# Optimization experiments

Measured on AMD Instinct MI355X. Metric: run time of the kernel, lower is better.

The kernel has to match this reference:

```python
import math
import jax, jax.numpy as jnp
import numpy as np

B, S, D = 16, 2048, 256

def setup_inputs() -> dict:
    key = jax.random.key(0)
    kq, kk, kv, km = jax.random.split(key, 4)
    q = jax.random.normal(kq, (B, S, D), dtype=jnp.float32)
    k = jax.random.normal(kk, (B, S, D), dtype=jnp.float32)
    v = jax.random.normal(kv, (B, S, D), dtype=jnp.float32)
    mask = jax.random.randint(km, (B, S, S), 0, 2, dtype=jnp.int32)
    return {"q": q, "k": k, "v": v, "mask": mask}

def reference(q, k, v, mask):
    dim_input = q.shape[-1]
    # scores: [B, S, S]
    scores = jnp.einsum('bqd,bkd->bqk', q, k) / math.sqrt(dim_input)
    # non-standard masking: masked positions set to 0.0 (NOT -inf) before softmax
    scores = jnp.where(mask == 0, jnp.float32(0.0), scores)
    att = jax.nn.softmax(scores, axis=-1)
    # original: if mask.sum() == 0, attention is all zeros
    att = jnp.where(mask.sum() > 0, att, jnp.zeros_like(att))
    return jnp.einsum('bqk,bkd->bqd', att, v)
```

## Files before the change

### kernel.cpp

```cpp
#include <hip/hip_runtime.h>


#define B_  16
#define S_  2048
#define D_  256
#define KT  32
#define NT_ 64
#define TILE_BYTES 16384

typedef short bf16x8 __attribute__((ext_vector_type(8)));
typedef float f32x4  __attribute__((ext_vector_type(4)));

__device__ __forceinline__ unsigned short f2bf(float x) {
    union { float f; unsigned u; } c; c.f = x;
    unsigned u = c.u;
    u += 0x7FFFu + ((u >> 16) & 1u);
    return (unsigned short)(u >> 16);
}

#define GLDS(g, l) __builtin_amdgcn_global_load_lds( \
    (const __attribute__((address_space(1))) void*)(g), \
    (__attribute__((address_space(3))) void*)(l), 16, 0, 0)

__global__ void conv_k(const float* __restrict__ k, char* __restrict__ kbf) {
    const int gid = blockIdx.x * 256 + threadIdx.x;
    const int d8  = gid & 31;
    const int kv  = (gid >> 5) & 2047;
    const int b   = gid >> 16;
    const float* src = k + (((size_t)(b * S_ + kv)) << 8) + d8 * 8;
    const float4 f0 = *(const float4*)src;
    const float4 f1 = *(const float4*)(src + 4);
    bf16x8 h;
    h[0] = (short)f2bf(f0.x); h[1] = (short)f2bf(f0.y);
    h[2] = (short)f2bf(f0.z); h[3] = (short)f2bf(f0.w);
    h[4] = (short)f2bf(f1.x); h[5] = (short)f2bf(f1.y);
    h[6] = (short)f2bf(f1.z); h[7] = (short)f2bf(f1.w);
    const int tile = kv >> 5, kvl = kv & 31;
    char* dst = kbf + (((size_t)(b * NT_ + tile)) << 14)
                    + (kvl << 9) + ((d8 * 16) ^ ((kvl & 7) << 4));
    *(bf16x8*)dst = h;
}

__global__ void conv_vt(const float* __restrict__ v, char* __restrict__ vtbf) {
    const int gid  = blockIdx.x * 256 + threadIdx.x;
    const int d    = gid & 255;
    const int g    = (gid >> 8) & 3;
    const int tile = (gid >> 10) & 63;
    const int b    = gid >> 16;
    const int kv0  = tile * KT + g * 8;
    const float* src = v + (((size_t)(b * S_ + kv0)) << 8) + d;
    bf16x8 h;
    #pragma unroll
    for (int j = 0; j < 8; ++j) h[j] = (short)f2bf(src[(size_t)j << 8]);
    char* dst = vtbf + (((size_t)(b * NT_ + tile)) << 14)
                     + (d << 6) + ((g * 16) ^ (((d >> 1) & 3) << 4));
    *(bf16x8*)dst = h;
}

__global__ __launch_bounds__(256, 1)
void attn_main(const float* __restrict__ q, const int* __restrict__ mask,
               const char* __restrict__ kbf, const char* __restrict__ vtbf,
               float* __restrict__ out)
{
    __shared__ alignas(128) char lds[73728];

    const int tid  = threadIdx.x;
    const int wid  = tid >> 6;
    const int lane = tid & 63;
    const int ln15 = lane & 15;
    const int quad = lane >> 4;
    const int swzK = (ln15 & 7) << 4;
    const int swzA = ((ln15 >> 1) & 3) << 4;

    const int bid = blockIdx.x;
    const int bx  = (bid & 7) * 32 + (bid >> 3);
    const int b   = bx >> 4;
    const int qt  = bx & 15;
    const int qw  = qt * 128 + wid * 32;

    const float QS = 0.09016844f;
    bf16x8 aq[2][8];
    #pragma unroll
    for (int s = 0; s < 2; ++s) {
        const float* qrow = q + ((size_t)(b * S_ + qw + s * 16 + ln15)) * D_;
        #pragma unroll
        for (int ks = 0; ks < 8; ++ks) {
            const float4 f0 = *(const float4*)(qrow + ks * 32 + quad * 8);
            const float4 f1 = *(const float4*)(qrow + ks * 32 + quad * 8 + 4);
            bf16x8 a;
            a[0] = (short)f2bf(f0.x * QS); a[1] = (short)f2bf(f0.y * QS);
            a[2] = (short)f2bf(f0.z * QS); a[3] = (short)f2bf(f0.w * QS);
            a[4] = (short)f2bf(f1.x * QS); a[5] = (short)f2bf(f1.y * QS);
            a[6] = (short)f2bf(f1.z * QS); a[7] = (short)f2bf(f1.w * QS);
            aq[s][ks] = a;
        }
    }

    bf16x8 ones;
    #pragma unroll
    for (int e = 0; e < 8; ++e) ones[e] = (short)0x3F80;

    f32x4 oacc[2][16];
    #pragma unroll
    for (int s = 0; s < 2; ++s)
        #pragma unroll
        for (int i = 0; i < 16; ++i) oacc[s][i] = (f32x4){0.f, 0.f, 0.f, 0.f};
    f32x4 lacc[2];
    lacc[0] = (f32x4){0.f, 0.f, 0.f, 0.f};
    lacc[1] = (f32x4){0.f, 0.f, 0.f, 0.f};

    const char* ktile = kbf  + (((size_t)b * NT_) << 14);
    const char* vtile = vtbf + (((size_t)b * NT_) << 14);
    char* pw = lds + 65536 + wid * 2048;
    const int c0 = wid * 4;

    #pragma unroll
    for (int c = 0; c < 4; ++c) {
        GLDS(ktile + (c0 + c) * 1024 + lane * 16, lds +         (c0 + c) * 1024);
        GLDS(vtile + (c0 + c) * 1024 + lane * 16, lds + 32768 + (c0 + c) * 1024);
    }

    const int* mbase = mask + ((size_t)(b * S_ + qw + 4 * quad)) * S_;
    int mcur[16], mnext[16];
    #pragma unroll
    for (int s = 0; s < 2; ++s)
        #pragma unroll
        for (int nt = 0; nt < 2; ++nt)
            #pragma unroll
            for (int r = 0; r < 4; ++r)
                mcur[s * 8 + nt * 4 + r] =
                    mbase[(size_t)(s * 16 + r) * S_ + nt * 16 + ln15];

    for (int t = 0; t < NT_; ++t) {
        const int cur = t & 1;
        __syncthreads();

        if (t + 1 < NT_) {
            const char* kg = ktile + ((size_t)(t + 1) << 14);
            const char* vg = vtile + ((size_t)(t + 1) << 14);
            const int nb = cur ^ 1;
            #pragma unroll
            for (int c = 0; c < 4; ++c) {
                GLDS(kg + (c0 + c) * 1024 + lane * 16, lds + nb * 16384 +         (c0 + c) * 1024);
                GLDS(vg + (c0 + c) * 1024 + lane * 16, lds + 32768 + nb * 16384 + (c0 + c) * 1024);
            }
            const int kv2 = (t + 1) * KT;
            #pragma unroll
            for (int s = 0; s < 2; ++s)
                #pragma unroll
                for (int nt = 0; nt < 2; ++nt)
                    #pragma unroll
                    for (int r = 0; r < 4; ++r)
                        mnext[s * 8 + nt * 4 + r] =
                            mbase[(size_t)(s * 16 + r) * S_ + kv2 + nt * 16 + ln15];
        }

        const char* kl = lds + cur * 16384;
        f32x4 sacc[2][2];
        sacc[0][0] = (f32x4){0.f, 0.f, 0.f, 0.f};
        sacc[0][1] = (f32x4){0.f, 0.f, 0.f, 0.f};
        sacc[1][0] = (f32x4){0.f, 0.f, 0.f, 0.f};
        sacc[1][1] = (f32x4){0.f, 0.f, 0.f, 0.f};
        #pragma unroll
        for (int ks = 0; ks < 8; ++ks) {
            #pragma unroll
            for (int nt = 0; nt < 2; ++nt) {
                const int off = ((nt * 16 + ln15) << 9)
                              + (((ks << 6) + (quad << 4)) ^ swzK);
                const bf16x8 bk = *(const bf16x8*)(kl + off);
                sacc[0][nt] = __builtin_amdgcn_mfma_f32_16x16x32_bf16(aq[0][ks], bk, sacc[0][nt], 0, 0, 0);
                sacc[1][nt] = __builtin_amdgcn_mfma_f32_16x16x32_bf16(aq[1][ks], bk, sacc[1][nt], 0, 0, 0);
            }
        }

        #pragma unroll
        for (int s = 0; s < 2; ++s) {
            #pragma unroll
            for (int nt = 0; nt < 2; ++nt) {
                #pragma unroll
                for (int r = 0; r < 4; ++r) {
                    const float p = (mcur[s * 8 + nt * 4 + r] != 0)
                                  ? exp2f(sacc[s][nt][r]) : 1.0f;
                    const int row  = s * 16 + 4 * quad + r;
                    const int boff = (row << 6)
                                   + ((nt * 32 + ln15 * 2) ^ (((row >> 1) & 3) << 4));
                    *(unsigned short*)(pw + boff) = f2bf(p);
                }
            }
        }

        const bf16x8 ap0 = *(const bf16x8*)(pw + (ln15 << 6)        + ((quad << 4) ^ swzA));
        const bf16x8 ap1 = *(const bf16x8*)(pw + ((16 + ln15) << 6) + ((quad << 4) ^ swzA));
        lacc[0] = __builtin_amdgcn_mfma_f32_16x16x32_bf16(ap0, ones, lacc[0], 0, 0, 0);
        lacc[1] = __builtin_amdgcn_mfma_f32_16x16x32_bf16(ap1, ones, lacc[1], 0, 0, 0);
        const char* vl = lds + 32768 + cur * 16384;
        #pragma unroll
        for (int nt2 = 0; nt2 < 16; ++nt2) {
            const int voff = ((nt2 * 16 + ln15) << 6) + ((quad << 4) ^ swzA);
            const bf16x8 bv = *(const bf16x8*)(vl + voff);
            oacc[0][nt2] = __builtin_amdgcn_mfma_f32_16x16x32_bf16(ap0, bv, oacc[0][nt2], 0, 0, 0);
            oacc[1][nt2] = __builtin_amdgcn_mfma_f32_16x16x32_bf16(ap1, bv, oacc[1][nt2], 0, 0, 0);
        }

        if (t + 1 < NT_) {
            #pragma unroll
            for (int i = 0; i < 16; ++i) mcur[i] = mnext[i];
        }
    }

    #pragma unroll
    for (int s = 0; s < 2; ++s) {
        #pragma unroll
        for (int r = 0; r < 4; ++r) {
            const float inv = 1.0f / lacc[s][r];
            float* orow = out + ((size_t)(b * S_ + qw + s * 16 + 4 * quad + r)) * D_ + ln15;
            #pragma unroll
            for (int nt2 = 0; nt2 < 16; ++nt2)
                orow[nt2 * 16] = oacc[s][nt2][r] * inv;
        }
    }
}

#define QT 128
#define KTF 64
#define NW 8
#define KSTR 264
#define VSTR 72
#define PSTR 72

__global__ __launch_bounds__(512, 2)
void attn_fused_v1(const float* __restrict__ q, const float* __restrict__ k,
                   const float* __restrict__ v, const int* __restrict__ mask,
                   float* __restrict__ out)
{
    __shared__ unsigned short Kl[KTF * KSTR];
    __shared__ unsigned short Vt[D_ * VSTR];
    __shared__ unsigned short Pl[NW][16 * PSTR];

    const int tid  = threadIdx.x;
    const int wid  = tid >> 6;
    const int lane = tid & 63;
    const int ln15 = lane & 15;
    const int quad = lane >> 4;
    const int bid = blockIdx.x;
    const int bx  = (bid & 7) * 32 + (bid >> 3);
    const int b  = bx >> 4;
    const int qt = bx & 15;
    const int qw = qt * QT + wid * 16;

    const float* qb = q + ((size_t)b * S_ + qw) * D_;
    const float* kb = k + (size_t)b * S_ * D_;
    const float* vb = v + (size_t)b * S_ * D_;
    const int*   mb = mask + ((size_t)b * S_ + qw) * (size_t)S_;

    bf16x8 aq[8];
    {
        const float* qrow = qb + (size_t)ln15 * D_;
        #pragma unroll
        for (int ks = 0; ks < 8; ++ks) {
            const float4 f0 = *(const float4*)(qrow + ks * 32 + quad * 8);
            const float4 f1 = *(const float4*)(qrow + ks * 32 + quad * 8 + 4);
            bf16x8 a;
            a[0] = (short)f2bf(f0.x * 0.0625f); a[1] = (short)f2bf(f0.y * 0.0625f);
            a[2] = (short)f2bf(f0.z * 0.0625f); a[3] = (short)f2bf(f0.w * 0.0625f);
            a[4] = (short)f2bf(f1.x * 0.0625f); a[5] = (short)f2bf(f1.y * 0.0625f);
            a[6] = (short)f2bf(f1.z * 0.0625f); a[7] = (short)f2bf(f1.w * 0.0625f);
            aq[ks] = a;
        }
    }
    bf16x8 ones;
    #pragma unroll
    for (int e = 0; e < 8; ++e) ones[e] = (short)0x3F80;
    f32x4 oacc[16];
    #pragma unroll
    for (int i = 0; i < 16; ++i) oacc[i] = (f32x4){0.f, 0.f, 0.f, 0.f};
    f32x4 lacc = (f32x4){0.f, 0.f, 0.f, 0.f};
    const int kst_c0 = (tid & 63) * 4;

    for (int kt2 = 0; kt2 < S_ / KTF; ++kt2) {
        const int kvbase = kt2 * KTF;
        int mval[4][4];
        #pragma unroll
        for (int nt = 0; nt < 4; ++nt)
            #pragma unroll
            for (int r = 0; r < 4; ++r)
                mval[nt][r] = mb[(size_t)(4 * quad + r) * S_ + kvbase + nt * 16 + ln15];
        __syncthreads();
        {
            const float* ks_ = kb + (size_t)kvbase * D_;
            #pragma unroll
            for (int pass = 0; pass < 8; ++pass) {
                const int r = pass * 8 + wid;
                const float4 f = *(const float4*)(ks_ + (size_t)r * D_ + kst_c0);
                ushort4 h;
                h.x = f2bf(f.x); h.y = f2bf(f.y); h.z = f2bf(f.z); h.w = f2bf(f.w);
                *(ushort4*)&Kl[r * KSTR + kst_c0] = h;
            }
        }
        {
            const float* vs_ = vb + (size_t)kvbase * D_;
            #pragma unroll
            for (int pass = 0; pass < 8; ++pass) {
                const int idx = pass * 8 + wid;
                const int kv  = (idx & 3) * 16 + ln15;
                const int d0  = (idx >> 2) * 16 + 4 * quad;
                const float4 f = *(const float4*)(vs_ + (size_t)kv * D_ + d0);
                Vt[(d0 + 0) * VSTR + kv] = f2bf(f.x);
                Vt[(d0 + 1) * VSTR + kv] = f2bf(f.y);
                Vt[(d0 + 2) * VSTR + kv] = f2bf(f.z);
                Vt[(d0 + 3) * VSTR + kv] = f2bf(f.w);
            }
        }
        __syncthreads();
        f32x4 sacc[4];
        #pragma unroll
        for (int nt = 0; nt < 4; ++nt) sacc[nt] = (f32x4){0.f, 0.f, 0.f, 0.f};
        #pragma unroll
        for (int ks = 0; ks < 8; ++ks) {
            #pragma unroll
            for (int nt = 0; nt < 4; ++nt) {
                const bf16x8 bk =
                    *(const bf16x8*)&Kl[(nt * 16 + ln15) * KSTR + ks * 32 + quad * 8];
                sacc[nt] = __builtin_amdgcn_mfma_f32_16x16x32_bf16(aq[ks], bk, sacc[nt], 0, 0, 0);
            }
        }
        unsigned short* pwv = Pl[wid];
        #pragma unroll
        for (int nt = 0; nt < 4; ++nt) {
            #pragma unroll
            for (int r = 0; r < 4; ++r) {
                const float s = sacc[nt][r];
                const float p = (mval[nt][r] != 0) ? __expf(s) : 1.0f;
                pwv[(4 * quad + r) * PSTR + nt * 16 + ln15] = f2bf(p);
            }
        }
        #pragma unroll
        for (int ks2 = 0; ks2 < 2; ++ks2) {
            const bf16x8 ap = *(const bf16x8*)&pwv[ln15 * PSTR + ks2 * 32 + quad * 8];
            lacc = __builtin_amdgcn_mfma_f32_16x16x32_bf16(ap, ones, lacc, 0, 0, 0);
            #pragma unroll
            for (int nt2 = 0; nt2 < 16; ++nt2) {
                const bf16x8 bv =
                    *(const bf16x8*)&Vt[(nt2 * 16 + ln15) * VSTR + ks2 * 32 + quad * 8];
                oacc[nt2] = __builtin_amdgcn_mfma_f32_16x16x32_bf16(ap, bv, oacc[nt2], 0, 0, 0);
            }
        }
    }
    #pragma unroll
    for (int r = 0; r < 4; ++r) {
        const float inv = 1.0f / lacc[r];
        float* orow = out + ((size_t)b * S_ + qw + 4 * quad + r) * D_ + ln15;
        #pragma unroll
        for (int nt2 = 0; nt2 < 16; ++nt2)
            orow[nt2 * 16] = oacc[nt2][r] * inv;
    }
}

extern "C" void kernel_launch(void* const* d_in, const int* in_sizes, int n_in,
                              void* d_out, int out_size, void* d_ws, size_t ws_size,
                              hipStream_t stream) {
    const float* q    = (const float*)d_in[0];
    const float* k    = (const float*)d_in[1];
    const float* v    = (const float*)d_in[2];
    const int*   mask = (const int*)d_in[3];
    float*       out  = (float*)d_out;

    const size_t one = (size_t)B_ * NT_ * TILE_BYTES;
    if (ws_size >= 2 * one) {
        char* kbf  = (char*)d_ws;
        char* vtbf = kbf + one;
        conv_k <<<4096, 256, 0, stream>>>(k, kbf);
        conv_vt<<<4096, 256, 0, stream>>>(v, vtbf);
        attn_main<<<256, 256, 0, stream>>>(q, mask, kbf, vtbf, out);
    } else {
        attn_fused_v1<<<512, 512, 0, stream>>>(q, k, v, mask, out);
    }
}
```

Before: 182.5 us.

## Split KV across two blocks, bit-pack mask, merge prep kernels, add reduce

New measurement: 311.2 us. +70.5%, slower.

```diff
diff --git a/kernel.cpp b/kernel.cpp
--- a/kernel.cpp
+++ b/kernel.cpp
@@ -4,8 +4,8 @@
 #define B_  16
 #define S_  2048
 #define D_  256
-#define KT  32
 #define NT_ 64
+#define NPH 32
 #define TILE_BYTES 16384
 
 typedef short bf16x8 __attribute__((ext_vector_type(8)));
@@ -22,45 +22,62 @@
     (const __attribute__((address_space(1))) void*)(g), \
     (__attribute__((address_space(3))) void*)(l), 16, 0, 0)
 
-__global__ void conv_k(const float* __restrict__ k, char* __restrict__ kbf) {
-    const int gid = blockIdx.x * 256 + threadIdx.x;
-    const int d8  = gid & 31;
-    const int kv  = (gid >> 5) & 2047;
-    const int b   = gid >> 16;
-    const float* src = k + (((size_t)(b * S_ + kv)) << 8) + d8 * 8;
-    const float4 f0 = *(const float4*)src;
-    const float4 f1 = *(const float4*)(src + 4);
-    bf16x8 h;
-    h[0] = (short)f2bf(f0.x); h[1] = (short)f2bf(f0.y);
-    h[2] = (short)f2bf(f0.z); h[3] = (short)f2bf(f0.w);
-    h[4] = (short)f2bf(f1.x); h[5] = (short)f2bf(f1.y);
-    h[6] = (short)f2bf(f1.z); h[7] = (short)f2bf(f1.w);
-    const int tile = kv >> 5, kvl = kv & 31;
-    char* dst = kbf + (((size_t)(b * NT_ + tile)) << 14)
-                    + (kvl << 9) + ((d8 * 16) ^ ((kvl & 7) << 4));
-    *(bf16x8*)dst = h;
-}
-
-__global__ void conv_vt(const float* __restrict__ v, char* __restrict__ vtbf) {
-    const int gid  = blockIdx.x * 256 + threadIdx.x;
-    const int d    = gid & 255;
-    const int g    = (gid >> 8) & 3;
-    const int tile = (gid >> 10) & 63;
-    const int b    = gid >> 16;
-    const int kv0  = tile * KT + g * 8;
-    const float* src = v + (((size_t)(b * S_ + kv0)) << 8) + d;
-    bf16x8 h;
-    #pragma unroll
-    for (int j = 0; j < 8; ++j) h[j] = (short)f2bf(src[(size_t)j << 8]);
-    char* dst = vtbf + (((size_t)(b * NT_ + tile)) << 14)
-                     + (d << 6) + ((g * 16) ^ (((d >> 1) & 3) << 4));
-    *(bf16x8*)dst = h;
-}
-
-__global__ __launch_bounds__(256, 1)
-void attn_main(const float* __restrict__ q, const int* __restrict__ mask,
-               const char* __restrict__ kbf, const char* __restrict__ vtbf,
-               float* __restrict__ out)
+__global__ __launch_bounds__(256)
+void prep_all(const float* __restrict__ k, const float* __restrict__ v,
+              const int* __restrict__ mask,
+              char* __restrict__ kbf, char* __restrict__ vtbf,
+              unsigned* __restrict__ pm)
+{
+    const int bid = blockIdx.x;
+    if (bid < 4096) {
+        const int gid = bid * 256 + threadIdx.x;
+        const int d8  = gid & 31;
+        const int kv  = (gid >> 5) & 2047;
+        const int b   = gid >> 16;
+        const float* src = k + (((size_t)(b * S_ + kv)) << 8) + d8 * 8;
+        const float4 f0 = *(const float4*)src;
+        const float4 f1 = *(const float4*)(src + 4);
+        bf16x8 h;
+        h[0] = (short)f2bf(f0.x); h[1] = (short)f2bf(f0.y);
+        h[2] = (short)f2bf(f0.z); h[3] = (short)f2bf(f0.w);
+        h[4] = (short)f2bf(f1.x); h[5] = (short)f2bf(f1.y);
+        h[6] = (short)f2bf(f1.z); h[7] = (short)f2bf(f1.w);
+        const int tile = kv >> 5, kvl = kv & 31;
+        char* dst = kbf + (((size_t)(b * NT_ + tile)) << 14)
+                        + (kvl << 9) + ((d8 * 16) ^ ((kvl & 7) << 4));
+        *(bf16x8*)dst = h;
+    } else if (bid < 8192) {
+        const int gid  = (bid - 4096) * 256 + threadIdx.x;
+        const int d    = gid & 255;
+        const int g    = (gid >> 8) & 3;
+        const int tile = (gid >> 10) & 63;
+        const int b    = gid >> 16;
+        const int kv0  = tile * 32 + g * 8;
+        const float* src = v + (((size_t)(b * S_ + kv0)) << 8) + d;
+        bf16x8 h;
+        #pragma unroll
+        for (int j = 0; j < 8; ++j) h[j] = (short)f2bf(src[(size_t)j << 8]);
+        char* dst = vtbf + (((size_t)(b * NT_ + tile)) << 14)
+                         + (d << 6) + ((g * 16) ^ (((d >> 1) & 3) << 4));
+        *(bf16x8*)dst = h;
+    } else {
+        const int wave = ((bid - 8192) * 256 + (int)threadIdx.x) >> 6;
+        const int lane = threadIdx.x & 63;
+        #pragma unroll 4
+        for (int it = 0; it < 32; ++it) {
+            const size_t grp = (size_t)it * 32768 + wave;
+            const int mv = mask[grp * 64 + lane];
+            const unsigned long long bal = __ballot(mv != 0);
+            if (lane == 0)      pm[grp * 2]     = (unsigned)bal;
+            else if (lane == 1) pm[grp * 2 + 1] = (unsigned)(bal >> 32);
+        }
+    }
+}
+
+__global__ __launch_bounds__(256, 2)
+void attn_split(const float* __restrict__ q, const unsigned* __restrict__ pm,
+                const char* __restrict__ kbf, const char* __restrict__ vtbf,
+                float* __restrict__ po, float* __restrict__ pl)
 {
     __shared__ alignas(128) char lds[73728];
 
@@ -73,9 +90,10 @@
     const int swzA = ((ln15 >> 1) & 3) << 4;
 
     const int bid = blockIdx.x;
-    const int bx  = (bid & 7) * 32 + (bid >> 3);
-    const int b   = bx >> 4;
-    const int qt  = bx & 15;
+    const int bx  = (bid & 7) * 64 + (bid >> 3);
+    const int b   = bx >> 5;
+    const int qt  = (bx >> 1) & 15;
+    const int hb  = bx & 1;
     const int qw  = qt * 128 + wid * 32;
 
     const float QS = 0.09016844f;
@@ -109,116 +127,138 @@
     lacc[0] = (f32x4){0.f, 0.f, 0.f, 0.f};
     lacc[1] = (f32x4){0.f, 0.f, 0.f, 0.f};
 
-    const char* ktile = kbf  + (((size_t)b * NT_) << 14);
-    const char* vtile = vtbf + (((size_t)b * NT_) << 14);
+    const char* ktile = kbf  + ((((size_t)b * NT_ + hb * 32)) << 14);
+    const char* vtile = vtbf + ((((size_t)b * NT_ + hb * 32)) << 14);
     char* pw = lds + 65536 + wid * 2048;
-    const int c0 = wid * 4;
+    const int cc = wid * 4;
 
     #pragma unroll
     for (int c = 0; c < 4; ++c) {
-        GLDS(ktile + (c0 + c) * 1024 + lane * 16, lds +         (c0 + c) * 1024);
-        GLDS(vtile + (c0 + c) * 1024 + lane * 16, lds + 32768 + (c0 + c) * 1024);
-    }
-
-    const int* mbase = mask + ((size_t)(b * S_ + qw + 4 * quad)) * S_;
-    int mcur[16], mnext[16];
+        GLDS(ktile + (cc + c) * 1024 + lane * 16, lds +         (cc + c) * 1024);
+        GLDS(vtile + (cc + c) * 1024 + lane * 16, lds + 32768 + (cc + c) * 1024);
+    }
+
+    const unsigned* pmrow = pm + ((size_t)(b * S_ + qw + 4 * quad)) * 64 + hb * 32;
+    unsigned mcur[8], mnext[8];
     #pragma unroll
     for (int s = 0; s < 2; ++s)
         #pragma unroll
-        for (int nt = 0; nt < 2; ++nt)
-            #pragma unroll
-            for (int r = 0; r < 4; ++r)
-                mcur[s * 8 + nt * 4 + r] =
-                    mbase[(size_t)(s * 16 + r) * S_ + nt * 16 + ln15];
-
-    for (int t = 0; t < NT_; ++t) {
-        const int cur = t & 1;
-        __syncthreads();
-
-        if (t + 1 < NT_) {
-            const char* kg = ktile + ((size_t)(t + 1) << 14);
-            const char* vg = vtile + ((size_t)(t + 1) << 14);
-            const int nb = cur ^ 1;
-            #pragma unroll
-            for (int c = 0; c < 4; ++c) {
-                GLDS(kg + (c0 + c) * 1024 + lane * 16, lds + nb * 16384 +         (c0 + c) * 1024);
-                GLDS(vg + (c0 + c) * 1024 + lane * 16, lds + 32768 + nb * 16384 + (c0 + c) * 1024);
-            }
-            const int kv2 = (t + 1) * KT;
-            #pragma unroll
-            for (int s = 0; s < 2; ++s)
-                #pragma unroll
-                for (int nt = 0; nt < 2; ++nt)
-                    #pragma unroll
-                    for (int r = 0; r < 4; ++r)
-                        mnext[s * 8 + nt * 4 + r] =
-                            mbase[(size_t)(s * 16 + r) * S_ + kv2 + nt * 16 + ln15];
-        }
-
-        const char* kl = lds + cur * 16384;
-        f32x4 sacc[2][2];
-        sacc[0][0] = (f32x4){0.f, 0.f, 0.f, 0.f};
-        sacc[0][1] = (f32x4){0.f, 0.f, 0.f, 0.f};
-        sacc[1][0] = (f32x4){0.f, 0.f, 0.f, 0.f};
-        sacc[1][1] = (f32x4){0.f, 0.f, 0.f, 0.f};
-        #pragma unroll
-        for (int ks = 0; ks < 8; ++ks) {
-            #pragma unroll
-            for (int nt = 0; nt < 2; ++nt) {
-                const int off = ((nt * 16 + ln15) << 9)
-                              + (((ks << 6) + (quad << 4)) ^ swzK);
-                const bf16x8 bk = *(const bf16x8*)(kl + off);
-                sacc[0][nt] = __builtin_amdgcn_mfma_f32_16x16x32_bf16(aq[0][ks], bk, sacc[0][nt], 0, 0, 0);
-                sacc[1][nt] = __builtin_amdgcn_mfma_f32_16x16x32_bf16(aq[1][ks], bk, sacc[1][nt], 0, 0, 0);
-            }
-        }
-
-        #pragma unroll
-        for (int s = 0; s < 2; ++s) {
-            #pragma unroll
-            for (int nt = 0; nt < 2; ++nt) {
-                #pragma unroll
-                for (int r = 0; r < 4; ++r) {
-                    const float p = (mcur[s * 8 + nt * 4 + r] != 0)
-                                  ? exp2f(sacc[s][nt][r]) : 1.0f;
-                    const int row  = s * 16 + 4 * quad + r;
-                    const int boff = (row << 6)
-                                   + ((nt * 32 + ln15 * 2) ^ (((row >> 1) & 3) << 4));
-                    *(unsigned short*)(pw + boff) = f2bf(p);
-                }
-            }
-        }
-
-        const bf16x8 ap0 = *(const bf16x8*)(pw + (ln15 << 6)        + ((quad << 4) ^ swzA));
-        const bf16x8 ap1 = *(const bf16x8*)(pw + ((16 + ln15) << 6) + ((quad << 4) ^ swzA));
-        lacc[0] = __builtin_amdgcn_mfma_f32_16x16x32_bf16(ap0, ones, lacc[0], 0, 0, 0);
-        lacc[1] = __builtin_amdgcn_mfma_f32_16x16x32_bf16(ap1, ones, lacc[1], 0, 0, 0);
-        const char* vl = lds + 32768 + cur * 16384;
-        #pragma unroll
-        for (int nt2 = 0; nt2 < 16; ++nt2) {
-            const int voff = ((nt2 * 16 + ln15) << 6) + ((quad << 4) ^ swzA);
-            const bf16x8 bv = *(const bf16x8*)(vl + voff);
-            oacc[0][nt2] = __builtin_amdgcn_mfma_f32_16x16x32_bf16(ap0, bv, oacc[0][nt2], 0, 0, 0);
-            oacc[1][nt2] = __builtin_amdgcn_mfma_f32_16x16x32_bf16(ap1, bv, oacc[1][nt2], 0, 0, 0);
-        }
-
-        if (t + 1 < NT_) {
-            #pragma unroll
-            for (int i = 0; i < 16; ++i) mcur[i] = mnext[i];
-        }
-    }
+        for (int r = 0; r < 4; ++r)
+            mcur[s * 4 + r] = pmrow[(size_t)(s * 16 + r) * 64];
+
+#define PHASE_BODY(T, CUR)                                                      \
+    {                                                                           \
+        __syncthreads();                                                        \
+        if ((T) + 1 < NPH) {                                                    \
+            const char* kg_ = ktile + ((size_t)((T) + 1) << 14);                \
+            const char* vg_ = vtile + ((size_t)((T) + 1) << 14);                \
+            _Pragma("unroll")                                                   \
+            for (int c = 0; c < 4; ++c) {                                       \
+                GLDS(kg_ + (cc + c) * 1024 + lane * 16,                         \
+                     lds + (CUR ^ 1) * 16384 +         (cc + c) * 1024);        \
+                GLDS(vg_ + (cc + c) * 1024 + lane * 16,                         \
+                     lds + 32768 + (CUR ^ 1) * 16384 + (cc + c) * 1024);        \
+            }                                                                   \
+            _Pragma("unroll")                                                   \
+            for (int s = 0; s < 2; ++s)                                         \
+                _Pragma("unroll")                                               \
+                for (int r = 0; r < 4; ++r)                                     \
+                    mnext[s * 4 + r] = pmrow[(size_t)(s * 16 + r) * 64 + (T) + 1]; \
+        }                                                                       \
+        const char* kl = lds + (CUR) * 16384;                                   \
+        f32x4 sacc[2][2];                                                       \
+        sacc[0][0] = (f32x4){0.f, 0.f, 0.f, 0.f};                               \
+        sacc[0][1] = (f32x4){0.f, 0.f, 0.f, 0.f};                               \
+        sacc[1][0] = (f32x4){0.f, 0.f, 0.f, 0.f};                               \
+        sacc[1][1] = (f32x4){0.f, 0.f, 0.f, 0.f};                               \
+        __builtin_amdgcn_s_setprio(1);                                          \
+        _Pragma("unroll")                                                       \
+        for (int ks = 0; ks < 8; ++ks) {                                        \
+            _Pragma("unroll")                                                   \
+            for (int nt = 0; nt < 2; ++nt) {                                    \
+                const int off = ((nt * 16 + ln15) << 9)                         \
+                              + (((ks << 6) + (quad << 4)) ^ swzK);             \
+                const bf16x8 bk = *(const bf16x8*)(kl + off);                   \
+                sacc[0][nt] = __builtin_amdgcn_mfma_f32_16x16x32_bf16(aq[0][ks], bk, sacc[0][nt], 0, 0, 0); \
+                sacc[1][nt] = __builtin_amdgcn_mfma_f32_16x16x32_bf16(aq[1][ks], bk, sacc[1][nt], 0, 0, 0); \
+            }                                                                   \
+        }                                                                       \
+        __builtin_amdgcn_s_setprio(0);                                          \
+        _Pragma("unroll")                                                       \
+        for (int s = 0; s < 2; ++s) {                                           \
+            _Pragma("unroll")                                                   \
+            for (int nt = 0; nt < 2; ++nt) {                                    \
+                _Pragma("unroll")                                               \
+                for (int r = 0; r < 4; ++r) {                                   \
+                    const float p = ((mcur[s * 4 + r] >> (nt * 16 + ln15)) & 1u) \
+                                  ? exp2f(sacc[s][nt][r]) : 1.0f;               \
+                    const int row  = s * 16 + 4 * quad + r;                     \
+                    const int boff = (row << 6)                                 \
+                                   + ((nt * 32 + ln15 * 2) ^ (((row >> 1) & 3) << 4)); \
+                    *(unsigned short*)(pw + boff) = f2bf(p);                    \
+                }                                                               \
+            }                                                                   \
+        }                                                                       \
+        const bf16x8 ap0 = *(const bf16x8*)(pw + (ln15 << 6)        + ((quad << 4) ^ swzA)); \
+        const bf16x8 ap1 = *(const bf16x8*)(pw + ((16 + ln15) << 6) + ((quad << 4) ^ swzA)); \
+        const char* vl = lds + 32768 + (CUR) * 16384;                           \
+        __builtin_amdgcn_s_setprio(1);                                          \
+        lacc[0] = __builtin_amdgcn_mfma_f32_16x16x32_bf16(ap0, ones, lacc[0], 0, 0, 0); \
+        lacc[1] = __builtin_amdgcn_mfma_f32_16x16x32_bf16(ap1, ones, lacc[1], 0, 0, 0); \
+        _Pragma("unroll")                                                       \
+        for (int nt2 = 0; nt2 < 16; ++nt2) {                                    \
+            const int voff = ((nt2 * 16 + ln15) << 6) + ((quad << 4) ^ swzA);   \
+            const bf16x8 bv = *(const bf16x8*)(vl + voff);                      \
+            oacc[0][nt2] = __builtin_amdgcn_mfma_f32_16x16x32_bf16(ap0, bv, oacc[0][nt2], 0, 0, 0); \
+            oacc[1][nt2] = __builtin_amdgcn_mfma_f32_16x16x32_bf16(ap1, bv, oacc[1][nt2], 0, 0, 0); \
+        }                                                                       \
+        __builtin_amdgcn_s_setprio(0);                                          \
+        if ((T) + 1 < NPH) {                                                    \
+            _Pragma("unroll")                                                   \
+            for (int i = 0; i < 8; ++i) mcur[i] = mnext[i];                     \
+        }                                                                       \
+    }
+
+    for (int t2 = 0; t2 < NPH / 2; ++t2) {
+        const int t = 2 * t2;
+        PHASE_BODY(t, 0);
+        PHASE_BODY(t + 1, 1);
+    }
+#undef PHASE_BODY
 
     #pragma unroll
     for (int s = 0; s < 2; ++s) {
         #pragma unroll
         for (int r = 0; r < 4; ++r) {
-            const float inv = 1.0f / lacc[s][r];
-            float* orow = out + ((size_t)(b * S_ + qw + s * 16 + 4 * quad + r)) * D_ + ln15;
+            const int gr = b * S_ + qw + s * 16 + 4 * quad + r;
+            float* prow = po + ((size_t)hb * (B_ * S_) + gr) * D_ + ln15;
             #pragma unroll
             for (int nt2 = 0; nt2 < 16; ++nt2)
-                orow[nt2 * 16] = oacc[s][nt2][r] * inv;
-        }
-    }
+                prow[nt2 * 16] = oacc[s][nt2][r];
+            if (ln15 == 0)
+                pl[(size_t)hb * (B_ * S_) + gr] = lacc[s][r];
+        }
+    }
+}
+
+__global__ __launch_bounds__(256)
+void reduce_o(const float* __restrict__ po, const float* __restrict__ pl,
+              float* __restrict__ out)
+{
+    const size_t gid  = (size_t)blockIdx.x * 256 + threadIdx.x;
+    const size_t base = gid * 8;
+    const size_t row  = base >> 8;
+    const float  l    = pl[row] + pl[(size_t)B_ * S_ + row];
+    const float  inv  = 1.0f / l;
+    const float4* a = (const float4*)(po + base);
+    const float4* c = (const float4*)(po + (size_t)B_ * S_ * D_ + base);
+    float4 r0, r1;
+    r0.x = (a[0].x + c[0].x) * inv; r0.y = (a[0].y + c[0].y) * inv;
+    r0.z = (a[0].z + c[0].z) * inv; r0.w = (a[0].w + c[0].w) * inv;
+    r1.x = (a[1].x + c[1].x) * inv; r1.y = (a[1].y + c[1].y) * inv;
+    r1.z = (a[1].z + c[1].z) * inv; r1.w = (a[1].w + c[1].w) * inv;
+    ((float4*)(out + base))[0] = r0;
+    ((float4*)(out + base))[1] = r1;
 }
 
 #define QT 128
@@ -292,9 +332,9 @@
             for (int pass = 0; pass < 8; ++pass) {
                 const int r = pass * 8 + wid;
                 const float4 f = *(const float4*)(ks_ + (size_t)r * D_ + kst_c0);
-                ushort4 h;
-                h.x = f2bf(f.x); h.y = f2bf(f.y); h.z = f2bf(f.z); h.w = f2bf(f.w);
-                *(ushort4*)&Kl[r * KSTR + kst_c0] = h;
+                ushort4 hh;
+                hh.x = f2bf(f.x); hh.y = f2bf(f.y); hh.z = f2bf(f.z); hh.w = f2bf(f.w);
+                *(ushort4*)&Kl[r * KSTR + kst_c0] = hh;
             }
         }
         {
@@ -365,14 +405,20 @@
     const int*   mask = (const int*)d_in[3];
     float*       out  = (float*)d_out;
 
-    const size_t one = (size_t)B_ * NT_ * TILE_BYTES;
-    if (ws_size >= 2 * one) {
-        char* kbf  = (char*)d_ws;
-        char* vtbf = kbf + one;
-        conv_k <<<4096, 256, 0, stream>>>(k, kbf);
-        conv_vt<<<4096, 256, 0, stream>>>(v, vtbf);
-        attn_main<<<256, 256, 0, stream>>>(q, mask, kbf, vtbf, out);
+    const size_t one  = (size_t)B_ * NT_ * TILE_BYTES;
+    const size_t pmsz = (size_t)B_ * S_ * 64 * 4;
+    const size_t posz = (size_t)2 * B_ * S_ * D_ * 4;
+    const size_t plsz = (size_t)2 * B_ * S_ * 4;
+    if (ws_size >= 2 * one + pmsz + posz + plsz) {
+        char*     kbf  = (char*)d_ws;
+        char*     vtbf = kbf + one;
+        unsigned* pmp  = (unsigned*)(vtbf + one);
+        float*    po   = (float*)((char*)pmp + pmsz);
+        float*    pl   = (float*)((char*)po + posz);
+        prep_all<<<16384, 256, 0, stream>>>(k, v, mask, kbf, vtbf, pmp);
+        attn_split<<<512, 256, 0, stream>>>(q, pmp, kbf, vtbf, po, pl);
+        reduce_o<<<4096, 256, 0, stream>>>(po, pl, out);
     } else {
-        attn_fused_v1<<<512, 512, 0, stream>>>(q, k, v, mask, out);
-    }
-}
+        attn_fused_v1<<<256, 512, 0, stream>>>(q, k, v, mask, out);
+    }
+}
```
